# Performance work log

Measured on AMD Instinct MI355X. Metric: run time of the kernel, lower is better.

## Reference

```python
import jax, jax.numpy as jnp
import numpy as np

B, N, K = 2, 2048, 30          # batch, residues, neighbors
DN, DE, L = 256, 128, 3        # dim_nodes, dim_edges, num_layers
NF, EF = 12, 28                # raw node / edge feature dims
EPS = 1e-6


def _gather(h, idx):
    # h: [B,N,D], idx: [B,N,K] -> [B,N,K,D]
    b, n, k = idx.shape
    d = h.shape[-1]
    return jnp.take_along_axis(h, idx.reshape(b, n * k, 1), axis=1).reshape(b, n, k, d)


def _nrm(v):
    return v / (jnp.linalg.norm(v, axis=-1, keepdims=True) + EPS)


def _forward(X, C, Wn, bn, We, be, Wm1, bm1, Wm2, bm2, Wue1, bue1, Wue2, bue2):
    mask_i = (C > 0).astype(X.dtype)                      # [B,N]
    Nat, CA, Cat, Oat = X[..., 0, :], X[..., 1, :], X[..., 2, :], X[..., 3, :]

    # local residue frames via Gram-Schmidt on (N, CA, C)
    u = _nrm(Cat - CA)
    v0 = Nat - CA
    v = _nrm(v0 - jnp.sum(v0 * u, -1, keepdims=True) * u)
    w = jnp.cross(u, v)
    R = jnp.stack([u, v, w], axis=-1)                     # [B,N,3,3]

    # node features: internal coords (unit bond vectors + log lengths)
    def bond_feat(bv):
        return jnp.concatenate([_nrm(bv), jnp.log(jnp.linalg.norm(bv, axis=-1, keepdims=True) + EPS)], -1)
    node_feat = jnp.concatenate([bond_feat(CA - Nat), bond_feat(Cat - CA), bond_feat(Oat - Cat)], -1)  # [B,N,12]
    node_h = (node_feat @ Wn + bn) * mask_i[..., None]

    # kNN graph on centroid distances (graph_distance_atom_type=-1)
    Xc = X.mean(axis=2)                                   # [B,N,3]
    D2 = jnp.sum((Xc[:, :, None] - Xc[:, None, :]) ** 2, -1)  # [B,N,N]
    BIG = 1e9
    D2 = D2 + BIG * (1.0 - mask_i)[:, None, :] + BIG * jnp.eye(N, dtype=X.dtype)[None]
    _, edge_idx = jax.lax.top_k(-D2, K)                   # [B,N,K]

    mask_j = _gather(mask_i[..., None], edge_idx)[..., 0]
    mask_ij = mask_i[..., None] * mask_j                  # [B,N,K]

    # edge features: RBF distances + local-frame direction + relative rotation
    xj = _gather(Xc, edge_idx)
    d = xj - Xc[:, :, None]                               # [B,N,K,3]
    dist = jnp.linalg.norm(d, axis=-1)
    local = jnp.einsum('bndc,bnkd->bnkc', R, d)           # R_i^T d
    dirv = local / (dist[..., None] + EPS)
    Rj = _gather(R.reshape(B, N, 9), edge_idx).reshape(B, N, K, 3, 3)
    Rrel = jnp.einsum('bnde,bnkdf->bnkef', R, Rj).reshape(B, N, K, 9)  # R_i^T R_j
    centers = jnp.linspace(0.0, 20.0, 16)
    sigma = 20.0 / 16.0
    rbf = jnp.exp(-(((dist[..., None] - centers) / sigma) ** 2))       # [B,N,K,16]
    edge_h = (jnp.concatenate([rbf, dirv, Rrel], -1) @ We + be) * mask_ij[..., None]

    # GNN message passing: gather -> MLP -> masked mean scatter, + edge update
    denom = jnp.sum(mask_ij, -1, keepdims=True) + EPS     # [B,N,1]
    for l in range(L):
        hj = _gather(node_h, edge_idx)                    # [B,N,K,DN]
        hi = jnp.broadcast_to(node_h[:, :, None], hj.shape)
        mi = jnp.concatenate([hi, hj, edge_h], -1)        # [B,N,K,2*DN+DE]
        m = jax.nn.softplus(mi @ Wm1[l] + bm1[l]) @ Wm2[l] + bm2[l]
        m = m * mask_ij[..., None]
        node_h = (node_h + m.sum(axis=2) / denom) * mask_i[..., None]
        e = jax.nn.softplus(mi @ Wue1[l] + bue1[l]) @ Wue2[l] + bue2[l]
        edge_h = (edge_h + e) * mask_ij[..., None]

    return node_h, edge_h, edge_idx, mask_i, mask_ij


def setup_inputs() -> dict:
    key = jax.random.key(0)
    ks = jax.random.split(key, 10)
    s = lambda i, shp: jax.random.normal(ks[i], shp, jnp.float32) * 0.05
    M = 2 * DN + DE
    inp = {
        'X': jax.random.normal(ks[0], (B, N, 4, 3), jnp.float32),
        'C': jax.random.randint(ks[1], (B, N), 0, 4),
        'Wn': s(2, (NF, DN)), 'bn': jnp.zeros((DN,), jnp.float32),
        'We': s(3, (EF, DE)), 'be': jnp.zeros((DE,), jnp.float32),
        'Wm1': s(4, (L, M, DN)), 'bm1': jnp.zeros((L, DN), jnp.float32),
        'Wm2': s(5, (L, DN, DN)), 'bm2': jnp.zeros((L, DN), jnp.float32),
        'Wue1': s(6, (L, M, DE)), 'bue1': jnp.zeros((L, DE), jnp.float32),
        'Wue2': s(7, (L, DE, DE)), 'bue2': jnp.zeros((L, DE), jnp.float32),
    }
    return inp


def reference(X, C, Wn, bn, We, be, Wm1, bm1, Wm2, bm2, Wue1, bue1, Wue2, bue2):
    return _forward(X, C, Wn, bn, We, be, Wm1, bm1, Wm2, bm2, Wue1, bue1, Wue2, bue2)
```

## Files before the change

kernel.cpp:

```cpp
#include <hip/hip_runtime.h>
#include <math.h>

#define Bdim 2
#define Nn   2048
#define Kn   30
#define KP   32
#define DNc  256
#define DEc  128
#define NODES (Bdim*Nn)
#define EDGES (Bdim*Nn*Kn)
#define RPAD  (NODES*KP)
#define EPSF 1e-6f

#define BK 64
#define LDA (BK+8)
#define LDA0 40
#define LDP 136

typedef __attribute__((ext_vector_type(8))) short short8;
typedef __attribute__((ext_vector_type(4))) short sh4;
typedef __attribute__((ext_vector_type(4))) float floatx4;

__device__ __forceinline__ float softplusf(float x){
    float e = __expf(-fabsf(x));
    return fmaxf(x, 0.f) + __logf(1.f + e);
}

__device__ __forceinline__ unsigned short f2bf(float x){
    union { float f; unsigned u; } v; v.f = x;
    unsigned r = v.u + 0x7fff + ((v.u >> 16) & 1);
    return (unsigned short)(r >> 16);
}
__device__ __forceinline__ float bf2f(unsigned short h){
    union { unsigned u; float f; } v; v.u = ((unsigned)h) << 16;
    return v.f;
}

__global__ __launch_bounds__(256) void k_geom(
    const float* __restrict__ X, const int* __restrict__ C,
    float* __restrict__ Xc, float* __restrict__ Rm,
    float* __restrict__ feat, float* __restrict__ mask_out)
{
    int id = blockIdx.x*256 + threadIdx.x;
    if (id >= NODES) return;
    float a[4][3];
    #pragma unroll
    for (int t=0;t<4;++t)
        #pragma unroll
        for (int d=0;d<3;++d) a[t][d] = X[id*12 + t*3 + d];
    #pragma unroll
    for (int d=0; d<3; ++d){
        float s = __fadd_rn(__fadd_rn(__fadd_rn(a[0][d],a[1][d]),a[2][d]),a[3][d]);
        Xc[id*3+d] = __fmul_rn(s, 0.25f);
    }
    mask_out[id] = (C[id] > 0) ? 1.f : 0.f;

    float u[3], v[3], w[3], b2[3], v0[3], vv[3];
    #pragma unroll
    for (int d=0;d<3;++d) b2[d] = a[2][d]-a[1][d];
    float n2 = sqrtf(b2[0]*b2[0]+b2[1]*b2[1]+b2[2]*b2[2]);
    #pragma unroll
    for (int d=0;d<3;++d) u[d] = b2[d]/(n2+EPSF);
    #pragma unroll
    for (int d=0;d<3;++d) v0[d] = a[0][d]-a[1][d];
    float dt = v0[0]*u[0]+v0[1]*u[1]+v0[2]*u[2];
    #pragma unroll
    for (int d=0;d<3;++d) vv[d] = v0[d] - dt*u[d];
    float nv = sqrtf(vv[0]*vv[0]+vv[1]*vv[1]+vv[2]*vv[2]);
    #pragma unroll
    for (int d=0;d<3;++d) v[d] = vv[d]/(nv+EPSF);
    w[0] = u[1]*v[2]-u[2]*v[1];
    w[1] = u[2]*v[0]-u[0]*v[2];
    w[2] = u[0]*v[1]-u[1]*v[0];
    #pragma unroll
    for (int d=0;d<3;++d){
        Rm[id*9 + d*3 + 0] = u[d];
        Rm[id*9 + d*3 + 1] = v[d];
        Rm[id*9 + d*3 + 2] = w[d];
    }
    float bonds[3][3];
    #pragma unroll
    for (int d=0;d<3;++d){
        bonds[0][d] = a[1][d]-a[0][d];
        bonds[1][d] = b2[d];
        bonds[2][d] = a[3][d]-a[2][d];
    }
    #pragma unroll
    for (int bi=0;bi<3;++bi){
        float nb = sqrtf(bonds[bi][0]*bonds[bi][0]+bonds[bi][1]*bonds[bi][1]+bonds[bi][2]*bonds[bi][2]);
        #pragma unroll
        for (int d=0;d<3;++d) feat[id*12 + bi*4 + d] = bonds[bi][d]/(nb+EPSF);
        feat[id*12 + bi*4 + 3] = logf(nb+EPSF);
    }
}

__global__ __launch_bounds__(256) void k_nodeh(
    const float* __restrict__ feat, const float* __restrict__ Wn,
    const float* __restrict__ bn, const int* __restrict__ C,
    float* __restrict__ node_h, unsigned short* __restrict__ node_bf)
{
    int nid = blockIdx.x;
    int c   = threadIdx.x;
    __shared__ float f[12];
    if (c < 12) f[c] = feat[nid*12 + c];
    __syncthreads();
    float acc = bn[c];
    #pragma unroll
    for (int k=0;k<12;++k) acc += f[k]*Wn[k*DNc + c];
    float mask = (C[nid] > 0) ? 1.f : 0.f;
    float r = acc*mask;
    node_h[nid*DNc + c] = r;
    node_bf[nid*DNc + c] = f2bf(r);
}

__global__ __launch_bounds__(256) void k_knn(
    const float* __restrict__ Xc, const int* __restrict__ C,
    int* __restrict__ eidx, float* __restrict__ eidx_f)
{
    __shared__ float sx[Nn], sy[Nn], sz[Nn], sadd[Nn];
    int tid  = threadIdx.x;
    int lane = tid & 63, wave = tid >> 6;
    int node0 = blockIdx.x*4;
    int base  = (node0 >> 11) << 11;
    for (int j=tid; j<Nn; j+=256){
        int gj = base + j;
        sx[j] = Xc[gj*3+0]; sy[j] = Xc[gj*3+1]; sz[j] = Xc[gj*3+2];
        sadd[j] = (C[gj] > 0) ? 0.f : 1e9f;
    }
    __syncthreads();

    int node = node0 + wave;
    int iloc = node & (Nn-1);
    float xi = sx[iloc], yi = sy[iloc], zi = sz[iloc];

    unsigned long long kreg[32];
    unsigned long long gm[8];
    #pragma unroll
    for (int t=0; t<32; ++t){
        int j = lane + t*64;
        float dx = __fsub_rn(xi, sx[j]);
        float dy = __fsub_rn(yi, sy[j]);
        float dz = __fsub_rn(zi, sz[j]);
        float vv = __fadd_rn(__fadd_rn(__fmul_rn(dx,dx),__fmul_rn(dy,dy)),__fmul_rn(dz,dz));
        vv = __fadd_rn(vv, sadd[j]);
        if (j == iloc) vv = __fadd_rn(vv, 1e9f);
        union { float f; unsigned u; } cv; cv.f = vv;
        kreg[t] = (((unsigned long long)cv.u) << 11) | (unsigned)j;
    }
    #pragma unroll
    for (int g=0; g<8; ++g){
        unsigned long long a = kreg[4*g+0], b = kreg[4*g+1];
        unsigned long long c = kreg[4*g+2], d = kreg[4*g+3];
        unsigned long long m1 = a<b?a:b, m2 = c<d?c:d;
        gm[g] = m1<m2?m1:m2;
    }
    unsigned long long m = gm[0]; int marg = 0;
    #pragma unroll
    for (int g=1; g<8; ++g) if (gm[g] < m){ m = gm[g]; marg = g; }

    for (int kk=0; kk<Kn; ++kk){
        unsigned long long best = m;
        #pragma unroll
        for (int d=1; d<64; d<<=1){
            unsigned long long o = __shfl_xor(best, d, 64);
            if (o < best) best = o;
        }
        if (lane == 0){
            int j = (int)(best & 2047ull);
            eidx  [(size_t)node*Kn + kk] = j;
            eidx_f[(size_t)node*Kn + kk] = (float)j;
        }
        if (m == best){
            #pragma unroll
            for (int g=0; g<8; ++g){
                if (marg == g){
                    #pragma unroll
                    for (int t=0; t<4; ++t)
                        if (kreg[4*g+t] == best) kreg[4*g+t] = ~0ull;
                    unsigned long long a = kreg[4*g+0], b = kreg[4*g+1];
                    unsigned long long c = kreg[4*g+2], d = kreg[4*g+3];
                    unsigned long long m1 = a<b?a:b, m2 = c<d?c:d;
                    gm[g] = m1<m2?m1:m2;
                }
            }
            m = gm[0]; marg = 0;
            #pragma unroll
            for (int g=1; g<8; ++g) if (gm[g] < m){ m = gm[g]; marg = g; }
        }
    }
}

__global__ __launch_bounds__(256) void k_edge_feat(
    const float* __restrict__ Xc, const float* __restrict__ Rm,
    const int* __restrict__ eidx, const int* __restrict__ C,
    unsigned short* __restrict__ featp,
    float* __restrict__ mask_ij_out, float* __restrict__ mask_pad,
    int* __restrict__ jg_pad, float* __restrict__ cnt)
{
    int r   = blockIdx.x*256 + threadIdx.x;
    int nid = r >> 5;
    int k   = r & 31;
    int b   = nid >> 11;
    float mij = 0.f;
    int   jb  = nid;
    float f[28];
    if (k < Kn){
        int e = nid*Kn + k;
        int j = eidx[e];
        jb = (b<<11) + j;
        mij = (C[nid] > 0 && C[jb] > 0) ? 1.f : 0.f;
        mask_ij_out[e] = mij;
        float xi0 = Xc[nid*3+0], xi1 = Xc[nid*3+1], xi2 = Xc[nid*3+2];
        float d0  = Xc[jb*3+0]-xi0;
        float d1  = Xc[jb*3+1]-xi1;
        float d2v = Xc[jb*3+2]-xi2;
        float dist = sqrtf(d0*d0 + d1*d1 + d2v*d2v);
        float ri[9], rj[9];
        #pragma unroll
        for (int q=0;q<9;++q) ri[q] = Rm[nid*9+q];
        #pragma unroll
        for (int q=0;q<9;++q) rj[q] = Rm[jb*9+q];
        #pragma unroll
        for (int c=0; c<16; ++c){
            float ctr = (20.f/15.f)*(float)c;
            float t = (dist - ctr)*(1.f/1.25f);
            f[c] = expf(-t*t);
        }
        #pragma unroll
        for (int cc=0; cc<3; ++cc){
            float loc = ri[0*3+cc]*d0 + ri[1*3+cc]*d1 + ri[2*3+cc]*d2v;
            f[16+cc] = loc/(dist+EPSF);
        }
        #pragma unroll
        for (int ee=0; ee<3; ++ee)
            #pragma unroll
            for (int ff=0; ff<3; ++ff)
                f[19+ee*3+ff] = ri[0+ee]*rj[0+ff] + ri[3+ee]*rj[3+ff] + ri[6+ee]*rj[6+ff];
    }
    jg_pad[r]   = jb;
    mask_pad[r] = mij;

    unsigned long long bal = __ballot(mij > 0.f);
    int lane = threadIdx.x & 63;
    if (lane == 0)  cnt[r >> 5] = (float)__popcll(bal & 0xFFFFFFFFull);
    if (lane == 32) cnt[r >> 5] = (float)__popcll(bal >> 32);

    unsigned short ov[32];
    #pragma unroll
    for (int q=0;q<32;++q) ov[q] = 0;
    if (k < Kn){
        #pragma unroll
        for (int q=0;q<28;++q) ov[q] = f2bf(f[q]);
    }
    unsigned short* dst = featp + (size_t)r*32;
    #pragma unroll
    for (int q=0; q<4; ++q){
        short8 sv;
        #pragma unroll
        for (int z=0; z<8; ++z) sv[z] = (short)ov[q*8+z];
        *(short8*)(dst + q*8) = sv;
    }
}

__global__ __launch_bounds__(256) void k_edge0(
    const unsigned short* __restrict__ featp, const unsigned short* __restrict__ Wp,
    const float* __restrict__ be, const float* __restrict__ mask_pad,
    unsigned short* __restrict__ edge_pad)
{
    __shared__ __align__(16) unsigned short smem[128*LDP];
    __shared__ float smask[128];
    unsigned short* Als  = smem;
    unsigned short* Bls  = smem + 128*LDA0;
    unsigned short* tile = smem;

    int tid = threadIdx.x;
    int lane = tid & 63, wave = tid >> 6;
    int wm = wave >> 1, wn = wave & 1;

    {
        const unsigned short* Ab = featp + (size_t)blockIdx.x*128*32;
        #pragma unroll
        for (int it=0; it<2; ++it){
            int idx = it*256 + tid;
            int row = idx >> 2, q = idx & 3;
            *(float4*)(&Als[row*LDA0 + q*8]) = *(const float4*)(Ab + row*32 + q*8);
        }
        if (tid < 128){
            int row = tid;
            *(float4*)(&Bls[row*LDA0 + 0])  = *(const float4*)(Wp + row*32 + 0);
            *(float4*)(&Bls[row*LDA0 + 8])  = *(const float4*)(Wp + row*32 + 8);
            *(float4*)(&Bls[row*LDA0 + 16]) = *(const float4*)(Wp + row*32 + 16);
            *(float4*)(&Bls[row*LDA0 + 24]) = *(const float4*)(Wp + row*32 + 24);
        } else {
            smask[tid-128] = mask_pad[blockIdx.x*128 + (tid-128)];
        }
    }
    __syncthreads();

    floatx4 acc[4][4];
    #pragma unroll
    for (int i=0;i<4;++i)
        #pragma unroll
        for (int j=0;j<4;++j) acc[i][j] = (floatx4){0.f,0.f,0.f,0.f};
    short8 af[4], bf[4];
    int kidx = (lane>>4)*8;
    #pragma unroll
    for (int t=0;t<4;++t){
        int row = wm*64 + t*16 + (lane&15);
        af[t] = *(const short8*)(&Als[row*LDA0 + kidx]);
        int col = wn*64 + t*16 + (lane&15);
        bf[t] = *(const short8*)(&Bls[col*LDA0 + kidx]);
    }
    __syncthreads();
    #pragma unroll
    for (int i=0;i<4;++i)
        #pragma unroll
        for (int j=0;j<4;++j)
            acc[i][j] = __builtin_amdgcn_mfma_f32_16x16x32_bf16(bf[j], af[i], acc[i][j], 0,0,0);

    int quad = lane >> 4, cl = lane & 15;
    #pragma unroll
    for (int i=0;i<4;++i){
        int rowl = wm*64 + i*16 + cl;
        float mk = smask[rowl];
        #pragma unroll
        for (int j=0;j<4;++j){
            int coll = wn*64 + j*16 + quad*4;
            float4 bv = *(const float4*)&be[coll];
            sh4 w;
            w[0] = (short)f2bf((acc[i][j][0] + bv.x)*mk);
            w[1] = (short)f2bf((acc[i][j][1] + bv.y)*mk);
            w[2] = (short)f2bf((acc[i][j][2] + bv.z)*mk);
            w[3] = (short)f2bf((acc[i][j][3] + bv.w)*mk);
            *(sh4*)(&tile[rowl*LDP + coll]) = w;
        }
    }
    __syncthreads();
    {
        int rl = tid >> 1;
        int h  = tid & 1;
        unsigned short* dst = edge_pad + (size_t)(blockIdx.x*128 + rl)*128 + h*64;
        #pragma unroll
        for (int q=0; q<8; ++q)
            *(short8*)(dst + q*8) = *(const short8*)(&tile[rl*LDP + h*64 + q*8]);
    }
}

__global__ __launch_bounds__(256) void k_pack_all(
    const float* __restrict__ We, const float* __restrict__ Wm1,
    const float* __restrict__ Wue1, const float* __restrict__ Wue2,
    const float* __restrict__ Wm2,
    unsigned short* __restrict__ wWe0, unsigned short* __restrict__ wPQw,
    unsigned short* __restrict__ wEw, unsigned short* __restrict__ wUe2w,
    unsigned short* __restrict__ wM2w)
{
    int id = blockIdx.x*256 + threadIdx.x;
    if (id < 4096){
        int n = id >> 5, kk = id & 31;
        wWe0[id] = (kk < 28) ? f2bf(We[kk*128 + n]) : 0;
        return;
    }
    id -= 4096;
    if (id < 3*768*256){
        int l = id / (768*256);
        int rem = id % (768*256);
        int n = rem >> 8, k = rem & 255;
        int c = (n < 384) ? n : n - 384;
        int r = (n < 384) ? k : 256 + k;
        float v = (c < 256) ? Wm1[((size_t)l*640 + r)*256 + c]
                            : Wue1[((size_t)l*640 + r)*128 + (c-256)];
        wPQw[id] = f2bf(v);
        return;
    }
    id -= 3*768*256;
    if (id < 3*384*128){
        int l = id / (384*128);
        int rem = id % (384*128);
        int n = rem >> 7, k = rem & 127;
        int r = 512 + k;
        float v = (n < 256) ? Wm1[((size_t)l*640 + r)*256 + n]
                            : Wue1[((size_t)l*640 + r)*128 + (n-256)];
        wEw[id] = f2bf(v);
        return;
    }
    id -= 3*384*128;
    if (id < 3*128*128){
        int l = id / (128*128);
        int rem = id % (128*128);
        int n = rem >> 7, k = rem & 127;
        wUe2w[id] = f2bf(Wue2[((size_t)l*128 + k)*128 + n]);
        return;
    }
    id -= 3*128*128;
    if (id < 3*256*256){
        int l = id / (256*256);
        int rem = id % (256*256);
        int n = rem >> 8, k = rem & 255;
        wM2w[id] = f2bf(Wm2[((size_t)l*256 + k)*256 + n]);
    }
}

template<int NR>
__device__ __forceinline__ void stage_tile_t(
    const unsigned short* __restrict__ gbase, int ldg, int k0,
    unsigned short* lds, int tid)
{
    #pragma unroll
    for (int it=0; it<NR/32; ++it){
        int idx = it*256 + tid;
        int row = idx >> 3;
        int ke  = (idx & 7) * 8;
        const float4* src = (const float4*)(gbase + (size_t)row*ldg + k0 + ke);
        *(float4*)(&lds[row*LDA + ke]) = *src;
    }
}

template<int TI, int TJ>
__device__ __forceinline__ void mma_tile_t(
    const unsigned short* Als, const unsigned short* Bls,
    int wm, int wn, int lane, floatx4 acc[TI][TJ])
{
    #pragma unroll
    for (int s=0; s<2; ++s){
        short8 af[TI], bf[TJ];
        int kidx = s*32 + (lane>>4)*8;
        #pragma unroll
        for (int t=0;t<TI;++t){
            int row = wm*(TI*16) + t*16 + (lane&15);
            af[t] = *(const short8*)(&Als[row*LDA + kidx]);
        }
        #pragma unroll
        for (int t=0;t<TJ;++t){
            int col = wn*(TJ*16) + t*16 + (lane&15);
            bf[t] = *(const short8*)(&Bls[col*LDA + kidx]);
        }
        #pragma unroll
        for (int i=0;i<TI;++i)
            #pragma unroll
            for (int j=0;j<TJ;++j)
                acc[i][j] = __builtin_amdgcn_mfma_f32_16x16x32_bf16(af[i], bf[j], acc[i][j], 0,0,0);
    }
}

template<int TI, int TJ>
__device__ __forceinline__ void mma_tile_sw(
    const unsigned short* Als, const unsigned short* Bls,
    int wm, int wn, int lane, floatx4 acc[TI][TJ])
{
    #pragma unroll
    for (int s=0; s<2; ++s){
        short8 af[TI], bf[TJ];
        int kidx = s*32 + (lane>>4)*8;
        #pragma unroll
        for (int t=0;t<TI;++t){
            int row = wm*(TI*16) + t*16 + (lane&15);
            af[t] = *(const short8*)(&Als[row*LDA + kidx]);
        }
        #pragma unroll
        for (int t=0;t<TJ;++t){
            int col = wn*(TJ*16) + t*16 + (lane&15);
            bf[t] = *(const short8*)(&Bls[col*LDA + kidx]);
        }
        #pragma unroll
        for (int i=0;i<TI;++i)
            #pragma unroll
            for (int j=0;j<TJ;++j)
                acc[i][j] = __builtin_amdgcn_mfma_f32_16x16x32_bf16(bf[j], af[i], acc[i][j], 0,0,0);
    }
}

__device__ __forceinline__ void mma_tileA_lp(
    const unsigned short* Atile, const unsigned short* Bls,
    int k0, int wm, int wn, int lane, floatx4 acc[4][4])
{
    #pragma unroll
    for (int s=0; s<2; ++s){
        short8 af[4], bf[4];
        int kloc = s*32 + (lane>>4)*8;
        #pragma unroll
        for (int t=0;t<4;++t){
            int row = wm*64 + t*16 + (lane&15);
            af[t] = *(const short8*)(&Atile[row*LDP + k0 + kloc]);
            int col = wn*64 + t*16 + (lane&15);
            bf[t] = *(const short8*)(&Bls[col*LDA + kloc]);
        }
        #pragma unroll
        for (int i=0;i<4;++i)
            #pragma unroll
            for (int j=0;j<4;++j)
                acc[i][j] = __builtin_amdgcn_mfma_f32_16x16x32_bf16(af[i], bf[j], acc[i][j], 0,0,0);
    }
}

__global__ __launch_bounds__(256) void k_pq(
    const unsigned short* __restrict__ A, const unsigned short* __restrict__ Bw,
    unsigned short* __restrict__ PQbf,
    const float* __restrict__ bm1l, const float* __restrict__ bue1l)
{
    __shared__ __align__(16) unsigned short smem[2*64*LDA];
    unsigned short* Als = smem;
    unsigned short* Bls = smem + 64*LDA;
    unsigned short* tile = smem;
    int tid = threadIdx.x;
    int lane = tid & 63, wave = tid >> 6;
    int wm = wave >> 1, wn = wave & 1;
    const unsigned short* Ab = A + (size_t)blockIdx.x*64*256;
    const unsigned short* Bb = Bw + (size_t)blockIdx.y*64*256;
    floatx4 acc[2][2];
    #pragma unroll
    for (int i=0;i<2;++i)
        #pragma unroll
        for (int j=0;j<2;++j) acc[i][j] = (floatx4){0.f,0.f,0.f,0.f};
    for (int k0=0; k0<256; k0+=BK){
        stage_tile_t<64>(Ab, 256, k0, Als, tid);
        stage_tile_t<64>(Bb, 256, k0, Bls, tid);
        __syncthreads();
        mma_tile_sw<2,2>(Als, Bls, wm, wn, lane, acc);
        __syncthreads();
    }
    int quad = lane >> 4, cl = lane & 15;
    #pragma unroll
    for (int i=0;i<2;++i){
        int rowl = wm*32 + i*16 + cl;
        #pragma unroll
        for (int j=0;j<2;++j){
            int coll = wn*32 + j*16 + quad*4;
            int col0 = blockIdx.y*64 + coll;
            float4 bv;
            if (col0 < 256)      bv = *(const float4*)&bm1l[col0];
            else if (col0 < 384) bv = *(const float4*)&bue1l[col0-256];
            else                 bv = (float4){0.f,0.f,0.f,0.f};
            sh4 w;
            w[0] = (short)f2bf(acc[i][j][0] + bv.x);
            w[1] = (short)f2bf(acc[i][j][1] + bv.y);
            w[2] = (short)f2bf(acc[i][j][2] + bv.z);
            w[3] = (short)f2bf(acc[i][j][3] + bv.w);
            *(sh4*)(&tile[rowl*LDP + coll]) = w;
        }
    }
    __syncthreads();
    {
        int rl = tid >> 2;
        int h  = tid & 3;
        unsigned short* dst = PQbf + (size_t)(blockIdx.x*64 + rl)*768 + blockIdx.y*64 + h*16;
        *(short8*)(dst + 0) = *(const short8*)(&tile[rl*LDP + h*16 + 0]);
        *(short8*)(dst + 8) = *(const short8*)(&tile[rl*LDP + h*16 + 8]);
    }
}

__global__ __launch_bounds__(256) void k_h1s(
    const unsigned short* __restrict__ Apad, const unsigned short* __restrict__ Bw,
    const unsigned short* __restrict__ PQbf, const int* __restrict__ jg_pad,
    const float* __restrict__ mask_pad,
    unsigned short* __restrict__ Sout)
{
    __shared__ __align__(16) unsigned short smem[2*128*LDA];
    __shared__ float smask[128];
    unsigned short* Als = smem;
    unsigned short* Bls = smem + 128*LDA;
    unsigned short* pqT = smem;

    int tid = threadIdx.x;
    int lane = tid & 63, wave = tid >> 6;
    int wm = wave >> 1, wn = wave & 1;
    int colblk = blockIdx.y;

    const unsigned short* Ab = Apad + (size_t)blockIdx.x*128*128;
    const unsigned short* Bb = Bw + (size_t)colblk*128*128;
    floatx4 acc[4][4];
    #pragma unroll
    for (int i=0;i<4;++i)
        #pragma unroll
        for (int j=0;j<4;++j) acc[i][j] = (floatx4){0.f,0.f,0.f,0.f};
    for (int k0=0; k0<128; k0+=BK){
        stage_tile_t<128>(Ab, 128, k0, Als, tid);
        stage_tile_t<128>(Bb, 128, k0, Bls, tid);
        __syncthreads();
        mma_tile_t<4,4>(Als, Bls, wm, wn, lane, acc);
        __syncthreads();
    }

    {
        int colbase = colblk*128;
        #pragma unroll
        for (int it=0; it<2; ++it){
            int w    = it*256 + tid;
            int rq   = w & 31;
            int c8   = w >> 5;
            int row0 = rq*4;
            int r0   = blockIdx.x*128 + row0;
            int ni   = r0 >> 5;
            int4 jg4 = *(const int4*)&jg_pad[r0];
            int colg = colbase + c8*8;
            short8 pv = *(const short8*)(PQbf + (size_t)ni*768 + colg);
            short8 q0 = *(const short8*)(PQbf + (size_t)jg4.x*768 + 384 + colg);
            short8 q1 = *(const short8*)(PQbf + (size_t)jg4.y*768 + 384 + colg);
            short8 q2 = *(const short8*)(PQbf + (size_t)jg4.z*768 + 384 + colg);
            short8 q3 = *(const short8*)(PQbf + (size_t)jg4.w*768 + 384 + colg);
            #pragma unroll
            for (int q=0; q<8; ++q){
                float pf = bf2f((unsigned short)pv[q]);
                sh4 ov;
                ov[0] = (short)f2bf(pf + bf2f((unsigned short)q0[q]));
                ov[1] = (short)f2bf(pf + bf2f((unsigned short)q1[q]));
                ov[2] = (short)f2bf(pf + bf2f((unsigned short)q2[q]));
                ov[3] = (short)f2bf(pf + bf2f((unsigned short)q3[q]));
                *(sh4*)(&pqT[(c8*8 + q)*LDP + row0]) = ov;
            }
        }
        if (tid < 128) smask[tid] = mask_pad[blockIdx.x*128 + tid];
    }
    __syncthreads();

    int quad = lane >> 4, cl = lane & 15;
    float sumA[4] = {0.f,0.f,0.f,0.f};
    float sumB[4] = {0.f,0.f,0.f,0.f};
    #pragma unroll
    for (int i=0;i<4;++i){
        int rowl0 = wm*64 + i*16 + quad*4;
        float4 mk = *(const float4*)&smask[rowl0];
        float mkv[4] = {mk.x, mk.y, mk.z, mk.w};
        #pragma unroll
        for (int j=0;j<4;++j){
            int coll = wn*64 + j*16 + cl;
            sh4 pq4 = *(const sh4*)(&pqT[coll*LDP + rowl0]);
            #pragma unroll
            for (int rg=0; rg<4; ++rg){
                float v  = softplusf(acc[i][j][rg] + bf2f((unsigned short)pq4[rg]));
                float mv = mkv[rg]*v;
                if (i < 2) sumA[j] += mv; else sumB[j] += mv;
            }
        }
    }

    int nodeA = blockIdx.x*4 + wm*2;
    #pragma unroll
    for (int j=0;j<4;++j){
        float a = sumA[j];
        a += __shfl_xor(a, 16, 64);
        a += __shfl_xor(a, 32, 64);
        float b = sumB[j];
        b += __shfl_xor(b, 16, 64);
        b += __shfl_xor(b, 32, 64);
        int col = colblk*128 + wn*64 + j*16 + cl;
        if (quad == 0)      Sout[(size_t)nodeA*256 + col]     = f2bf(a);
        else if (quad == 1) Sout[(size_t)(nodeA+1)*256 + col] = f2bf(b);
    }
}

__global__ __launch_bounds__(256) void k_h1e(
    const unsigned short* __restrict__ Apad, const unsigned short* __restrict__ BwE,
    const unsigned short* __restrict__ BwU2,
    const unsigned short* __restrict__ PQbf, const int* __restrict__ jg_pad,
    const float* __restrict__ mask_pad, const float* __restrict__ bue2l,
    unsigned short* __restrict__ edge_pad, float* __restrict__ edge_f32,
    int last)
{
    __shared__ __align__(16) unsigned short smem[26624];
    unsigned short* Als  = smem;
    unsigned short* Bls  = smem + 128*LDA;
    unsigned short* tile = smem;
    unsigned short* B2   = smem + 128*LDP;

    int tid = threadIdx.x;
    int lane = tid & 63, wave = tid >> 6;
    int wm = wave >> 1, wn = wave & 1;

    const unsigned short* Ab = Apad + (size_t)blockIdx.x*128*128;
    floatx4 acc[4][4];
    #pragma unroll
    for (int i=0;i<4;++i)
        #pragma unroll
        for (int j=0;j<4;++j) acc[i][j] = (floatx4){0.f,0.f,0.f,0.f};
    for (int k0=0; k0<128; k0+=BK){
        stage_tile_t<128>(Ab, 128, k0, Als, tid);
        stage_tile_t<128>(BwE, 128, k0, Bls, tid);
        __syncthreads();
        mma_tile_t<4,4>(Als, Bls, wm, wn, lane, acc);
        __syncthreads();
    }

    stage_tile_t<128>(BwU2, 128, 0, B2, tid);

    {
        int rl = tid >> 1;
        int h  = tid & 1;
        int r  = blockIdx.x*128 + rl;
        int ni = r >> 5;
        int jg = jg_pad[r];
        int cb = 256 + h*64;
        const unsigned short* Pr = PQbf + (size_t)ni*768 + cb;
        const unsigned short* Qr = PQbf + (size_t)jg*768 + 384 + cb;
        #pragma unroll
        for (int q=0; q<8; ++q){
            short8 pv = *(const short8*)(Pr + q*8);
            short8 qv = *(const short8*)(Qr + q*8);
            short8 ov;
            #pragma unroll
            for (int z=0; z<8; ++z)
                ov[z] = (short)f2bf(bf2f((unsigned short)pv[z]) + bf2f((unsigned short)qv[z]));
            *(short8*)(&tile[rl*LDP + h*64 + q*8]) = ov;
        }
    }
    __syncthreads();

    int quad = lane >> 4, cl = lane & 15;
    #pragma unroll
    for (int i=0;i<4;++i){
        #pragma unroll
        for (int rg=0;rg<4;++rg){
            int rowl = wm*64 + i*16 + quad*4 + rg;
            #pragma unroll
            for (int j=0;j<4;++j){
                int coll = wn*64 + j*16 + cl;
                float pq = bf2f(tile[rowl*LDP + coll]);
                float v  = softplusf(acc[i][j][rg] + pq);
                tile[rowl*LDP + coll] = f2bf(v);
            }
        }
    }
    __syncthreads();

    floatx4 acc2[4][4];
    #pragma unroll
    for (int i=0;i<4;++i)
        #pragma unroll
        for (int j=0;j<4;++j) acc2[i][j] = (floatx4){0.f,0.f,0.f,0.f};
    mma_tileA_lp(tile, B2, 0, wm, wn, lane, acc2);
    __syncthreads();
    stage_tile_t<128>(BwU2, 128, 64, B2, tid);
    __syncthreads();
    mma_tileA_lp(tile, B2, 64, wm, wn, lane, acc2);
    __syncthreads();

    float* sbias = (float*)B2;
    #pragma unroll
    for (int i=0;i<4;++i){
        #pragma unroll
        for (int rg=0;rg<4;++rg){
            int rowl = wm*64 + i*16 + quad*4 + rg;
            #pragma unroll
            for (int j=0;j<4;++j){
                int coll = wn*64 + j*16 + cl;
                tile[rowl*LDP + coll] = f2bf(acc2[i][j][rg]);
            }
        }
    }
    if (tid < 128) sbias[tid] = bue2l[tid];
    __syncthreads();

    if (last){
        int c16  = lane & 31;
        int rsub = lane >> 5;
        #pragma unroll
        for (int step=0; step<16; ++step){
            int rowl = wave*32 + step*2 + rsub;
            int R = blockIdx.x*128 + rowl;
            int k = R & (KP-1);
            if (k < Kn){
                float mij = mask_pad[R];
                int node = R >> 5;
                int e = node*Kn + k;
                sh4 ov = *(const sh4*)(edge_pad + (size_t)R*128 + c16*4);
                sh4 av = *(const sh4*)(&tile[rowl*LDP + c16*4]);
                float4 bv = *(const float4*)(&sbias[c16*4]);
                float4 f;
                f.x = (bf2f((unsigned short)ov[0]) + bf2f((unsigned short)av[0]) + bv.x)*mij;
                f.y = (bf2f((unsigned short)ov[1]) + bf2f((unsigned short)av[1]) + bv.y)*mij;
                f.z = (bf2f((unsigned short)ov[2]) + bf2f((unsigned short)av[2]) + bv.z)*mij;
                f.w = (bf2f((unsigned short)ov[3]) + bf2f((unsigned short)av[3]) + bv.w)*mij;
                *(float4*)(edge_f32 + (size_t)e*128 + c16*4) = f;
            }
        }
    } else {
        int c8   = lane & 15;
        int rsub = lane >> 4;
        #pragma unroll
        for (int step=0; step<8; ++step){
            int rowl = wave*32 + step*4 + rsub;
            int R = blockIdx.x*128 + rowl;
            int k = R & (KP-1);
            if (k < Kn){
                float mij = mask_pad[R];
                unsigned short* ep = edge_pad + (size_t)R*128 + c8*8;
                short8 ov = *(const short8*)ep;
                short8 av = *(const short8*)(&tile[rowl*LDP + c8*8]);
                float4 b0 = *(const float4*)(&sbias[c8*8]);
                float4 b1 = *(const float4*)(&sbias[c8*8 + 4]);
                float nv[8];
                nv[0] = (bf2f((unsigned short)ov[0]) + bf2f((unsigned short)av[0]) + b0.x)*mij;
                nv[1] = (bf2f((unsigned short)ov[1]) + bf2f((unsigned short)av[1]) + b0.y)*mij;
                nv[2] = (bf2f((unsigned short)ov[2]) + bf2f((unsigned short)av[2]) + b0.z)*mij;
                nv[3] = (bf2f((unsigned short)ov[3]) + bf2f((unsigned short)av[3]) + b0.w)*mij;
                nv[4] = (bf2f((unsigned short)ov[4]) + bf2f((unsigned short)av[4]) + b1.x)*mij;
                nv[5] = (bf2f((unsigned short)ov[5]) + bf2f((unsigned short)av[5]) + b1.y)*mij;
                nv[6] = (bf2f((unsigned short)ov[6]) + bf2f((unsigned short)av[6]) + b1.z)*mij;
                nv[7] = (bf2f((unsigned short)ov[7]) + bf2f((unsigned short)av[7]) + b1.w)*mij;
                short8 sv;
                #pragma unroll
                for (int z=0; z<8; ++z) sv[z] = (short)f2bf(nv[z]);
                *(short8*)ep = sv;
            }
        }
    }
}

__global__ __launch_bounds__(256) void k_node_gemm(
    const unsigned short* __restrict__ S, const unsigned short* __restrict__ Bw,
    const float* __restrict__ bm2l, const float* __restrict__ cnt,
    const float* __restrict__ mask_i,
    float* __restrict__ node_h, unsigned short* __restrict__ node_bf)
{
    __shared__ __align__(16) unsigned short Als[32*LDA];
    __shared__ __align__(16) unsigned short Bls[64*LDA];
    int tid = threadIdx.x;
    int lane = tid & 63, wave = tid >> 6;
    int wm = wave >> 1, wn = wave & 1;
    const unsigned short* Ab = S + (size_t)blockIdx.x*32*256;
    const unsigned short* Bb = Bw + (size_t)blockIdx.y*64*256;
    floatx4 acc[1][2];
    acc[0][0] = (floatx4){0.f,0.f,0.f,0.f};
    acc[0][1] = (floatx4){0.f,0.f,0.f,0.f};
    for (int k0=0; k0<256; k0+=BK){
        stage_tile_t<32>(Ab, 256, k0, Als, tid);
        stage_tile_t<64>(Bb, 256, k0, Bls, tid);
        __syncthreads();
        mma_tile_sw<1,2>(Als, Bls, wm, wn, lane, acc);
        __syncthreads();
    }
    int quad = lane >> 4, cl = lane & 15;
    {
        int nid = blockIdx.x*32 + wm*16 + cl;
        float ct = cnt[nid];
        float mi = mask_i[nid];
        float dv = ct + EPSF;
        #pragma unroll
        for (int j=0;j<2;++j){
            int col = blockIdx.y*64 + wn*32 + j*16 + quad*4;
            float4 bv = *(const float4*)&bm2l[col];
            float4 nh = *(const float4*)&node_h[(size_t)nid*256 + col];
            float4 r;
            r.x = (nh.x + (acc[0][j][0] + ct*bv.x)/dv)*mi;
            r.y = (nh.y + (acc[0][j][1] + ct*bv.y)/dv)*mi;
            r.z = (nh.z + (acc[0][j][2] + ct*bv.z)/dv)*mi;
            r.w = (nh.w + (acc[0][j][3] + ct*bv.w)/dv)*mi;
            *(float4*)&node_h[(size_t)nid*256 + col] = r;
            sh4 w;
            w[0] = (short)f2bf(r.x);
            w[1] = (short)f2bf(r.y);
            w[2] = (short)f2bf(r.z);
            w[3] = (short)f2bf(r.w);
            *(sh4*)&node_bf[(size_t)nid*256 + col] = w;
        }
    }
}

extern "C" void kernel_launch(void* const* d_in, const int* in_sizes, int n_in,
                              void* d_out, int out_size, void* d_ws, size_t ws_size,
                              hipStream_t stream)
{
    (void)in_sizes; (void)n_in; (void)out_size; (void)ws_size;
    const float* X   = (const float*)d_in[0];
    const int*   C   = (const int*)  d_in[1];
    const float* Wn  = (const float*)d_in[2];
    const float* bn  = (const float*)d_in[3];
    const float* We  = (const float*)d_in[4];
    const float* be  = (const float*)d_in[5];
    const float* Wm1 = (const float*)d_in[6];
    const float* bm1 = (const float*)d_in[7];
    const float* Wm2 = (const float*)d_in[8];
    const float* bm2 = (const float*)d_in[9];
    const float* Wue1= (const float*)d_in[10];
    const float* bue1= (const float*)d_in[11];
    const float* Wue2= (const float*)d_in[12];
    const float* bue2= (const float*)d_in[13];

    float* out       = (float*)d_out;
    float* out_node  = out;
    float* out_edge  = out + 1048576;
    float* out_eidxf = out + 16777216;
    float* out_maski = out + 16900096;
    float* out_maskij= out + 16904192;

    char* wsb = (char*)d_ws;
    size_t off = 0;
    float* wXc    = (float*)(wsb + off); off += (size_t)12288*4;
    float* wR     = (float*)(wsb + off); off += (size_t)36864*4;
    float* wF     = (float*)(wsb + off); off += (size_t)49152*4;
    int*   wEidx  = (int*)  (wsb + off); off += (size_t)EDGES*4;
    int*   wJgPad = (int*)  (wsb + off); off += (size_t)RPAD*4;
    float* wMaskP = (float*)(wsb + off); off += (size_t)RPAD*4;
    float* wCnt   = (float*)(wsb + off); off += (size_t)NODES*4;
    unsigned short* wPQ      = (unsigned short*)(wsb + off); off += (size_t)NODES*768*2;
    unsigned short* wS       = (unsigned short*)(wsb + off); off += (size_t)NODES*256*2;
    unsigned short* wNodeBf  = (unsigned short*)(wsb + off); off += (size_t)NODES*256*2;
    unsigned short* wEdgePad = (unsigned short*)(wsb + off); off += (size_t)RPAD*128*2;
    unsigned short* wFeatP   = (unsigned short*)(wsb + off); off += (size_t)RPAD*32*2;
    unsigned short* wWe0     = (unsigned short*)(wsb + off); off += (size_t)128*32*2;
    unsigned short* wPQw     = (unsigned short*)(wsb + off); off += (size_t)3*768*256*2;
    unsigned short* wEw      = (unsigned short*)(wsb + off); off += (size_t)3*384*128*2;
    unsigned short* wUe2w    = (unsigned short*)(wsb + off); off += (size_t)3*128*128*2;
    unsigned short* wM2w     = (unsigned short*)(wsb + off); off += (size_t)3*256*256*2;

    k_geom <<<16,    256, 0, stream>>>(X, C, wXc, wR, wF, out_maski);
    k_nodeh<<<NODES, 256, 0, stream>>>(wF, Wn, bn, C, out_node, wNodeBf);
    k_knn  <<<NODES/4, 256, 0, stream>>>(wXc, C, wEidx, out_eidxf);

    k_pack_all<<<3856, 256, 0, stream>>>(We, Wm1, Wue1, Wue2, Wm2,
                                         wWe0, wPQw, wEw, wUe2w, wM2w);
    k_edge_feat<<<RPAD/256, 256, 0, stream>>>(wXc, wR, wEidx, C, wFeatP,
                                              out_maskij, wMaskP, wJgPad, wCnt);
    k_edge0<<<RPAD/128, 256, 0, stream>>>(wFeatP, wWe0, be, wMaskP, wEdgePad);

    for (int l=0; l<3; ++l){
        k_pq<<<dim3(64,12), 256, 0, stream>>>(wNodeBf, wPQw + (size_t)l*768*256, wPQ,
                                              bm1 + l*256, bue1 + l*128);
        k_h1s<<<dim3(RPAD/128,2), 256, 0, stream>>>(
            wEdgePad, wEw + (size_t)l*384*128, wPQ, wJgPad, wMaskP, wS);
        k_h1e<<<RPAD/128, 256, 0, stream>>>(
            wEdgePad, wEw + (size_t)l*384*128 + (size_t)256*128,
            wUe2w + (size_t)l*128*128, wPQ, wJgPad, wMaskP, bue2 + l*128,
            wEdgePad, out_edge, (l==2) ? 1 : 0);
        k_node_gemm<<<dim3(NODES/32,4), 256, 0, stream>>>(
            wS, wM2w + (size_t)l*256*256, bm2 + l*256, wCnt, out_maski,
            out_node, wNodeBf);
    }
}
```

Before: 443.8 us.

## Shrink k_h1e shared memory by processing edge update in two 64-column halves

Restructures the fused edge-update kernel so the P+Q gather, softplus and second GEMM are done in two 64-column halves that reuse the same A/B staging buffers. The full 128x136 tile buffer goes away, and bias moves to its own small array. This reduces LDS per block from about 52KB to about 37KB, which allows more resident blocks per CU. The price is extra barriers, only half the waves doing softplus and writeback in each phase, and a serialized writeback per half.

```diff
diff --git a/kernel.cpp b/kernel.cpp
--- a/kernel.cpp
+++ b/kernel.cpp
@@ -469,29 +469,6 @@
     }
 }
 
-__device__ __forceinline__ void mma_tileA_lp(
-    const unsigned short* Atile, const unsigned short* Bls,
-    int k0, int wm, int wn, int lane, floatx4 acc[4][4])
-{
-    #pragma unroll
-    for (int s=0; s<2; ++s){
-        short8 af[4], bf[4];
-        int kloc = s*32 + (lane>>4)*8;
-        #pragma unroll
-        for (int t=0;t<4;++t){
-            int row = wm*64 + t*16 + (lane&15);
-            af[t] = *(const short8*)(&Atile[row*LDP + k0 + kloc]);
-            int col = wn*64 + t*16 + (lane&15);
-            bf[t] = *(const short8*)(&Bls[col*LDA + kloc]);
-        }
-        #pragma unroll
-        for (int i=0;i<4;++i)
-            #pragma unroll
-            for (int j=0;j<4;++j)
-                acc[i][j] = __builtin_amdgcn_mfma_f32_16x16x32_bf16(af[i], bf[j], acc[i][j], 0,0,0);
-    }
-}
-
 __global__ __launch_bounds__(256) void k_pq(
     const unsigned short* __restrict__ A, const unsigned short* __restrict__ Bw,
     unsigned short* __restrict__ PQbf,
@@ -656,15 +633,17 @@
     unsigned short* __restrict__ edge_pad, float* __restrict__ edge_f32,
     int last)
 {
-    __shared__ __align__(16) unsigned short smem[26624];
-    unsigned short* Als  = smem;
-    unsigned short* Bls  = smem + 128*LDA;
-    unsigned short* tile = smem;
-    unsigned short* B2   = smem + 128*LDP;
+    __shared__ __align__(16) unsigned short smem[2*128*LDA];
+    __shared__ float sbias[128];
+    unsigned short* Als = smem;
+    unsigned short* Bls = smem + 128*LDA;
 
     int tid = threadIdx.x;
     int lane = tid & 63, wave = tid >> 6;
     int wm = wave >> 1, wn = wave & 1;
+    int quad = lane >> 4, cl = lane & 15;
+
+    if (tid < 128) sbias[tid] = bue2l[tid];
 
     const unsigned short* Ab = Apad + (size_t)blockIdx.x*128*128;
     floatx4 acc[4][4];
@@ -680,113 +659,89 @@
         __syncthreads();
     }
 
-    stage_tile_t<128>(BwU2, 128, 0, B2, tid);
-
-    {
-        int rl = tid >> 1;
-        int h  = tid & 1;
-        int r  = blockIdx.x*128 + rl;
-        int ni = r >> 5;
-        int jg = jg_pad[r];
-        int cb = 256 + h*64;
-        const unsigned short* Pr = PQbf + (size_t)ni*768 + cb;
-        const unsigned short* Qr = PQbf + (size_t)jg*768 + 384 + cb;
-        #pragma unroll
-        for (int q=0; q<8; ++q){
-            short8 pv = *(const short8*)(Pr + q*8);
-            short8 qv = *(const short8*)(Qr + q*8);
-            short8 ov;
-            #pragma unroll
-            for (int z=0; z<8; ++z)
-                ov[z] = (short)f2bf(bf2f((unsigned short)pv[z]) + bf2f((unsigned short)qv[z]));
-            *(short8*)(&tile[rl*LDP + h*64 + q*8]) = ov;
-        }
-    }
-    __syncthreads();
-
-    int quad = lane >> 4, cl = lane & 15;
-    #pragma unroll
-    for (int i=0;i<4;++i){
-        #pragma unroll
-        for (int rg=0;rg<4;++rg){
-            int rowl = wm*64 + i*16 + quad*4 + rg;
-            #pragma unroll
-            for (int j=0;j<4;++j){
-                int coll = wn*64 + j*16 + cl;
-                float pq = bf2f(tile[rowl*LDP + coll]);
-                float v  = softplusf(acc[i][j][rg] + pq);
-                tile[rowl*LDP + coll] = f2bf(v);
+    int rl   = tid >> 1;
+    int hsub = tid & 1;
+    int r    = blockIdx.x*128 + rl;
+    int ni   = r >> 5;
+    int jg   = jg_pad[r];
+
+    floatx4 acc2[4][4];
+    #pragma unroll
+    for (int i=0;i<4;++i)
+        #pragma unroll
+        for (int j=0;j<4;++j) acc2[i][j] = (floatx4){0.f,0.f,0.f,0.f};
+
+    #pragma unroll
+    for (int h=0; h<2; ++h){
+        {
+            int cb = 256 + h*64 + hsub*32;
+            const unsigned short* Pr = PQbf + (size_t)ni*768 + cb;
+            const unsigned short* Qr = PQbf + (size_t)jg*768 + 384 + cb;
+            #pragma unroll
+            for (int q=0; q<4; ++q){
+                short8 pv = *(const short8*)(Pr + q*8);
+                short8 qv = *(const short8*)(Qr + q*8);
+                short8 ov;
+                #pragma unroll
+                for (int z=0; z<8; ++z)
+                    ov[z] = (short)f2bf(bf2f((unsigned short)pv[z]) + bf2f((unsigned short)qv[z]));
+                *(short8*)(&Als[rl*LDA + hsub*32 + q*8]) = ov;
             }
         }
-    }
-    __syncthreads();
-
-    floatx4 acc2[4][4];
-    #pragma unroll
-    for (int i=0;i<4;++i)
-        #pragma unroll
-        for (int j=0;j<4;++j) acc2[i][j] = (floatx4){0.f,0.f,0.f,0.f};
-    mma_tileA_lp(tile, B2, 0, wm, wn, lane, acc2);
-    __syncthreads();
-    stage_tile_t<128>(BwU2, 128, 64, B2, tid);
-    __syncthreads();
-    mma_tileA_lp(tile, B2, 64, wm, wn, lane, acc2);
-    __syncthreads();
-
-    float* sbias = (float*)B2;
-    #pragma unroll
-    for (int i=0;i<4;++i){
-        #pragma unroll
-        for (int rg=0;rg<4;++rg){
-            int rowl = wm*64 + i*16 + quad*4 + rg;
-            #pragma unroll
-            for (int j=0;j<4;++j){
-                int coll = wn*64 + j*16 + cl;
-                tile[rowl*LDP + coll] = f2bf(acc2[i][j][rg]);
+        stage_tile_t<128>(BwU2, 128, h*64, Bls, tid);
+        __syncthreads();
+
+        if (wn == h){
+            #pragma unroll
+            for (int i=0;i<4;++i){
+                #pragma unroll
+                for (int rg=0;rg<4;++rg){
+                    int rowl = wm*64 + i*16 + quad*4 + rg;
+                    #pragma unroll
+                    for (int j=0;j<4;++j){
+                        int c = j*16 + cl;
+                        float pq = bf2f(Als[rowl*LDA + c]);
+                        Als[rowl*LDA + c] = f2bf(softplusf(acc[i][j][rg] + pq));
+                    }
+                }
             }
         }
-    }
-    if (tid < 128) sbias[tid] = bue2l[tid];
-    __syncthreads();
-
-    if (last){
-        int c16  = lane & 31;
-        int rsub = lane >> 5;
-        #pragma unroll
-        for (int step=0; step<16; ++step){
-            int rowl = wave*32 + step*2 + rsub;
-            int R = blockIdx.x*128 + rowl;
-            int k = R & (KP-1);
-            if (k < Kn){
-                float mij = mask_pad[R];
-                int node = R >> 5;
-                int e = node*Kn + k;
-                sh4 ov = *(const sh4*)(edge_pad + (size_t)R*128 + c16*4);
-                sh4 av = *(const sh4*)(&tile[rowl*LDP + c16*4]);
-                float4 bv = *(const float4*)(&sbias[c16*4]);
-                float4 f;
-                f.x = (bf2f((unsigned short)ov[0]) + bf2f((unsigned short)av[0]) + bv.x)*mij;
-                f.y = (bf2f((unsigned short)ov[1]) + bf2f((unsigned short)av[1]) + bv.y)*mij;
-                f.z = (bf2f((unsigned short)ov[2]) + bf2f((unsigned short)av[2]) + bv.z)*mij;
-                f.w = (bf2f((unsigned short)ov[3]) + bf2f((unsigned short)av[3]) + bv.w)*mij;
-                *(float4*)(edge_f32 + (size_t)e*128 + c16*4) = f;
+        __syncthreads();
+
+        mma_tile_t<4,4>(Als, Bls, wm, wn, lane, acc2);
+        __syncthreads();
+    }
+
+    int kk = r & (KP-1);
+    float mij = mask_pad[r];
+    int node = r >> 5;
+    int e = node*Kn + kk;
+    #pragma unroll
+    for (int h=0; h<2; ++h){
+        if (wn == h){
+            #pragma unroll
+            for (int i=0;i<4;++i){
+                #pragma unroll
+                for (int rg=0;rg<4;++rg){
+                    int rowl = wm*64 + i*16 + quad*4 + rg;
+                    #pragma unroll
+                    for (int j=0;j<4;++j){
+                        int c = j*16 + cl;
+                        Als[rowl*LDA + c] = f2bf(acc2[i][j][rg]);
+                    }
+                }
             }
         }
-    } else {
-        int c8   = lane & 15;
-        int rsub = lane >> 4;
-        #pragma unroll
-        for (int step=0; step<8; ++step){
-            int rowl = wave*32 + step*4 + rsub;
-            int R = blockIdx.x*128 + rowl;
-            int k = R & (KP-1);
-            if (k < Kn){
-                float mij = mask_pad[R];
-                unsigned short* ep = edge_pad + (size_t)R*128 + c8*8;
-                short8 ov = *(const short8*)ep;
-                short8 av = *(const short8*)(&tile[rowl*LDP + c8*8]);
-                float4 b0 = *(const float4*)(&sbias[c8*8]);
-                float4 b1 = *(const float4*)(&sbias[c8*8 + 4]);
+        __syncthreads();
+        if (kk < Kn){
+            #pragma unroll
+            for (int q=0; q<4; ++q){
+                int c = hsub*32 + q*8;
+                const unsigned short* op = edge_pad + (size_t)r*128 + h*64 + c;
+                short8 ov = *(const short8*)op;
+                short8 av = *(const short8*)(&Als[rl*LDA + c]);
+                float4 b0 = *(const float4*)(&sbias[h*64 + c]);
+                float4 b1 = *(const float4*)(&sbias[h*64 + c + 4]);
                 float nv[8];
                 nv[0] = (bf2f((unsigned short)ov[0]) + bf2f((unsigned short)av[0]) + b0.x)*mij;
                 nv[1] = (bf2f((unsigned short)ov[1]) + bf2f((unsigned short)av[1]) + b0.y)*mij;
@@ -796,12 +751,21 @@
                 nv[5] = (bf2f((unsigned short)ov[5]) + bf2f((unsigned short)av[5]) + b1.y)*mij;
                 nv[6] = (bf2f((unsigned short)ov[6]) + bf2f((unsigned short)av[6]) + b1.z)*mij;
                 nv[7] = (bf2f((unsigned short)ov[7]) + bf2f((unsigned short)av[7]) + b1.w)*mij;
-                short8 sv;
-                #pragma unroll
-                for (int z=0; z<8; ++z) sv[z] = (short)f2bf(nv[z]);
-                *(short8*)ep = sv;
+                if (last){
+                    float4 f0 = {nv[0],nv[1],nv[2],nv[3]};
+                    float4 f1 = {nv[4],nv[5],nv[6],nv[7]};
+                    float* fp = edge_f32 + (size_t)e*128 + h*64 + c;
+                    *(float4*)(fp)     = f0;
+                    *(float4*)(fp + 4) = f1;
+                } else {
+                    short8 sv;
+                    #pragma unroll
+                    for (int z=0; z<8; ++z) sv[z] = (short)f2bf(nv[z]);
+                    *(short8*)(edge_pad + (size_t)r*128 + h*64 + c) = sv;
+                }
             }
         }
+        if (h == 0) __syncthreads();
     }
 }
 
```

New measurement: 557.3 us. 1.26x slower.
